# Kernel optimization log

Measured on AMD Instinct MI355X. Metric: run time of the kernel, lower is better.

## Reference

```python
import jax, jax.numpy as jnp
import numpy as np

IN_F = 4096
OUT_F = 4096
K = 16
THRESH = 0.0


def _group_ids():
    # consecutive chunks of size q = IN_F // K; last chunk absorbs remainder
    q, r = IN_F // K, IN_F % K
    ids = np.concatenate([np.full(q, k, np.int32) for k in range(K - 1)]
                         + [np.full(q + r, K - 1, np.int32)])
    return jnp.asarray(ids)


def setup_inputs() -> dict:
    key = jax.random.key(0)
    k1, k2, k3 = jax.random.split(key, 3)
    bound = 1.0 / np.sqrt(IN_F)
    x = jax.random.normal(k1, (8, 2048, IN_F), dtype=jnp.float32)
    weight = jax.random.uniform(k2, (OUT_F, IN_F), jnp.float32, -bound, bound)
    bias = jax.random.uniform(k3, (OUT_F,), jnp.float32, -bound, bound)
    return {"x": x, "weight": weight, "bias": bias}


def reference(x, weight, bias):
    B, T, F = x.shape
    xf = x.reshape(-1, F)                       # [N, F]
    # sum over output units of W @ x_chunk == colsum(W) . x_chunk
    wsum = jnp.sum(weight, axis=0)              # [F]
    contrib = xf * wsum[None, :]                # [N, F]
    gids = _group_ids()
    # group sums: [K, N] -> [N, K]
    g = jax.ops.segment_sum(contrib.T, gids, num_segments=K).T
    cs = jnp.cumsum(g, axis=1)                  # prefix activations [N, K]
    hit = cs >= THRESH
    idx = jnp.where(jnp.any(hit, axis=1), jnp.argmax(hit, axis=1), K - 1)
    S = jnp.take_along_axis(cs, idx[:, None], axis=1)  # [N, 1] scalar activation
    out = jax.nn.sigmoid(S + bias[None, :])     # [N, OUT_F]
    return out.reshape(B, T, OUT_F)
```

## Files before the change

### kernel.cpp

```cpp
#include <hip/hip_runtime.h>

#define IN_F 4096
#define OUT_F 4096
#define KGRP 16
#define N_ROWS (8 * 2048)
#define RPB 8
#define NBLK (N_ROWS / RPB)
#define WPARTS 32

typedef float f32x4 __attribute__((ext_vector_type(4)));


__global__ __launch_bounds__(256) void wsum_partial_kernel(const float* __restrict__ w,
                                                           double* __restrict__ partial) {
    const int f = blockIdx.x * 256 + threadIdx.x;
    const int r0 = blockIdx.y * (OUT_F / WPARTS);
    const float* p = w + (size_t)r0 * IN_F + f;
    double s = 0.0;
#pragma unroll 16
    for (int o = 0; o < OUT_F / WPARTS; ++o) s += (double)p[(size_t)o * IN_F];
    partial[blockIdx.y * IN_F + f] = s;
}

__global__ __launch_bounds__(256) void wsum_reduce_kernel(const double* __restrict__ partial,
                                                          double* __restrict__ wsum) {
    const int f = blockIdx.x * 256 + threadIdx.x;
    double s = 0.0;
#pragma unroll
    for (int p = 0; p < WPARTS; ++p) s += partial[p * IN_F + f];
    wsum[f] = s;
}

__global__ __launch_bounds__(256) void srow_kernel(const float* __restrict__ x,
                                                   const double* __restrict__ wsum,
                                                   float* __restrict__ S) {
    const int t = threadIdx.x;
    const int lane = t & 63;
    const int wave = t >> 6;
    const int n0 = blockIdx.x * RPB;

    __shared__ double g[RPB][KGRP];

    double wreg[16];
#pragma unroll
    for (int k = 0; k < 4; ++k) {
        const double* wp = &wsum[4 * (k * 256 + t)];
        double2 w01 = *(const double2*)(wp);
        double2 w23 = *(const double2*)(wp + 2);
        wreg[4 * k + 0] = w01.x; wreg[4 * k + 1] = w01.y;
        wreg[4 * k + 2] = w23.x; wreg[4 * k + 3] = w23.y;
    }

    for (int r = 0; r < RPB; ++r) {
        const f32x4* xr = (const f32x4*)(x + (size_t)(n0 + r) * IN_F);
        double part[4];
#pragma unroll
        for (int k = 0; k < 4; ++k) {
            f32x4 v = __builtin_nontemporal_load(&xr[k * 256 + t]);
            part[k] = (double)v.x * wreg[4 * k + 0] + (double)v.y * wreg[4 * k + 1] +
                      (double)v.z * wreg[4 * k + 2] + (double)v.w * wreg[4 * k + 3];
        }
        {
            double keep01 = (lane & 1) ? part[1] : part[0];
            double send01 = (lane & 1) ? part[0] : part[1];
            double keep23 = (lane & 1) ? part[3] : part[2];
            double send23 = (lane & 1) ? part[2] : part[3];
            double w01 = keep01 + __shfl_xor(send01, 1, 64);
            double w23 = keep23 + __shfl_xor(send23, 1, 64);
            double keep = (lane & 2) ? w23 : w01;
            double send = (lane & 2) ? w01 : w23;
            double rv = keep + __shfl_xor(send, 2, 64);
#pragma unroll
            for (int off = 4; off <= 32; off <<= 1)
                rv += __shfl_xor(rv, off, 64);
            if (lane < 4) g[r][lane * 4 + wave] = rv;
        }
    }
    __syncthreads();

    if (t < RPB) {
        double cs = 0.0, Sv = 0.0;
        bool found = false;
#pragma unroll
        for (int k = 0; k < KGRP; ++k) {
            cs += g[t][k];
            if (!found && cs >= 0.0) { Sv = cs; found = true; }
        }
        if (!found) Sv = cs;
        S[n0 + t] = (float)Sv;
    }
}

__global__ __launch_bounds__(256) void out_kernel(const float* __restrict__ S,
                                                  const float* __restrict__ bias,
                                                  float* __restrict__ out) {
    const int t = threadIdx.x;
    const int n0 = blockIdx.x * RPB;
    const f32x4* b4 = (const f32x4*)bias;

    f32x4 b[4];
#pragma unroll
    for (int k = 0; k < 4; ++k) b[k] = b4[k * 256 + t];

    for (int r = 0; r < RPB; ++r) {
        const float Sv = S[n0 + r];
        f32x4* o4 = (f32x4*)(out + (size_t)(n0 + r) * OUT_F);
#pragma unroll
        for (int k = 0; k < 4; ++k) {
            f32x4 rr;
            rr.x = __builtin_amdgcn_rcpf(1.0f + __expf(-(Sv + b[k].x)));
            rr.y = __builtin_amdgcn_rcpf(1.0f + __expf(-(Sv + b[k].y)));
            rr.z = __builtin_amdgcn_rcpf(1.0f + __expf(-(Sv + b[k].z)));
            rr.w = __builtin_amdgcn_rcpf(1.0f + __expf(-(Sv + b[k].w)));
            __builtin_nontemporal_store(rr, &o4[k * 256 + t]);
        }
    }
}

extern "C" void kernel_launch(void* const* d_in, const int* in_sizes, int n_in,
                              void* d_out, int out_size, void* d_ws, size_t ws_size,
                              hipStream_t stream) {
    const float* x    = (const float*)d_in[0];
    const float* w    = (const float*)d_in[1];
    const float* bias = (const float*)d_in[2];
    float* out = (float*)d_out;

    char* ws = (char*)d_ws;
    double* wsum    = (double*)(ws);
    float*  S       = (float*)(ws + 32 * 1024);
    double* partial = (double*)(ws + 96 * 1024);

    dim3 g1(IN_F / 256, WPARTS);
    wsum_partial_kernel<<<g1, 256, 0, stream>>>(w, partial);
    wsum_reduce_kernel<<<IN_F / 256, 256, 0, stream>>>(partial, wsum);
    srow_kernel<<<NBLK, 256, 0, stream>>>(x, wsum, S);
    out_kernel<<<NBLK, 256, 0, stream>>>(S, bias, out);
}
```

Measured before the change: 122.2 us.

## Restructure weight column-sum into row-blocked vectorized partials with wide reduction

The weight column-sum pass changes from a 2D grid of scalar strided loads over 32 row partitions to 256 blocks. Each block reads 16 full rows with nontemporal float4 loads and keeps 16 double accumulators per thread. The aim is wider, streaming reads of the weight matrix. In exchange the partial buffer grows to 256×4096 doubles, and the reduce kernel must sum 256 partials per column with only 16 blocks, which may be latency-bound and may exceed the workspace layout. The row loop in srow_kernel also gets an unroll-by-2 hint.

```diff
diff --git a/kernel.cpp b/kernel.cpp
--- a/kernel.cpp
+++ b/kernel.cpp
@@ -6,28 +6,48 @@
 #define N_ROWS (8 * 2048)
 #define RPB 8
 #define NBLK (N_ROWS / RPB)
-#define WPARTS 32
+#define WROWS 16
+#define WBLKS (OUT_F / WROWS)
 
 typedef float f32x4 __attribute__((ext_vector_type(4)));
 
 
 __global__ __launch_bounds__(256) void wsum_partial_kernel(const float* __restrict__ w,
                                                            double* __restrict__ partial) {
-    const int f = blockIdx.x * 256 + threadIdx.x;
-    const int r0 = blockIdx.y * (OUT_F / WPARTS);
-    const float* p = w + (size_t)r0 * IN_F + f;
-    double s = 0.0;
-#pragma unroll 16
-    for (int o = 0; o < OUT_F / WPARTS; ++o) s += (double)p[(size_t)o * IN_F];
-    partial[blockIdx.y * IN_F + f] = s;
+    const int t = threadIdx.x;
+    const f32x4* wr = (const f32x4*)(w + (size_t)blockIdx.x * WROWS * IN_F);
+
+    double acc[16];
+#pragma unroll
+    for (int i = 0; i < 16; ++i) acc[i] = 0.0;
+
+#pragma unroll 4
+    for (int o = 0; o < WROWS; ++o) {
+#pragma unroll
+        for (int c = 0; c < 4; ++c) {
+            f32x4 v = __builtin_nontemporal_load(&wr[o * (IN_F / 4) + c * 256 + t]);
+            acc[4 * c + 0] += (double)v.x;
+            acc[4 * c + 1] += (double)v.y;
+            acc[4 * c + 2] += (double)v.z;
+            acc[4 * c + 3] += (double)v.w;
+        }
+    }
+
+    double* pr = partial + (size_t)blockIdx.x * IN_F;
+#pragma unroll
+    for (int c = 0; c < 4; ++c) {
+        double2* pp = (double2*)&pr[4 * (c * 256 + t)];
+        pp[0] = make_double2(acc[4 * c + 0], acc[4 * c + 1]);
+        pp[1] = make_double2(acc[4 * c + 2], acc[4 * c + 3]);
+    }
 }
 
 __global__ __launch_bounds__(256) void wsum_reduce_kernel(const double* __restrict__ partial,
                                                           double* __restrict__ wsum) {
     const int f = blockIdx.x * 256 + threadIdx.x;
     double s = 0.0;
-#pragma unroll
-    for (int p = 0; p < WPARTS; ++p) s += partial[p * IN_F + f];
+#pragma unroll 8
+    for (int p = 0; p < WBLKS; ++p) s += partial[(size_t)p * IN_F + f];
     wsum[f] = s;
 }
 
@@ -51,6 +71,7 @@
         wreg[4 * k + 2] = w23.x; wreg[4 * k + 3] = w23.y;
     }
 
+#pragma unroll 2
     for (int r = 0; r < RPB; ++r) {
         const f32x4* xr = (const f32x4*)(x + (size_t)(n0 + r) * IN_F);
         double part[4];
@@ -130,8 +151,7 @@
     float*  S       = (float*)(ws + 32 * 1024);
     double* partial = (double*)(ws + 96 * 1024);
 
-    dim3 g1(IN_F / 256, WPARTS);
-    wsum_partial_kernel<<<g1, 256, 0, stream>>>(w, partial);
+    wsum_partial_kernel<<<WBLKS, 256, 0, stream>>>(w, partial);
     wsum_reduce_kernel<<<IN_F / 256, 256, 0, stream>>>(partial, wsum);
     srow_kernel<<<NBLK, 256, 0, stream>>>(x, wsum, S);
     out_kernel<<<NBLK, 256, 0, stream>>>(S, bias, out);
```

New measurement: 131.5 us. 7.6% more time.
